# Kernel tuning notes

Measured on AMD Instinct MI355X. Metric: run time of the kernel, lower is better.

## Reference

```python
import jax, jax.numpy as jnp
import numpy as np

B, L, H, D = 2, 2048, 16, 64
HID = H * D
EPS = 1e-6


def setup_inputs() -> dict:
    key = jax.random.key(0)
    k1, k2, k3 = jax.random.split(key, 3)
    x = jax.random.normal(k1, (B, L, HID), dtype=jnp.float32)
    Wqkv = jax.random.normal(k2, (HID, 3 * HID), dtype=jnp.float32) * 0.02
    Wo = jax.random.normal(k3, (HID, HID), dtype=jnp.float32) * 0.02
    q_norm_w = jnp.ones((D,), dtype=jnp.float32)
    k_norm_w = jnp.ones((D,), dtype=jnp.float32)
    # real RoPE tables: (L, D/2)
    d2 = D // 2
    inv_freq = 1.0 / (10000.0 ** (np.arange(d2, dtype=np.float32) / d2))
    ang = np.arange(L, dtype=np.float32)[:, None] * inv_freq[None, :]
    cos = jnp.asarray(np.cos(ang), dtype=jnp.float32)
    sin = jnp.asarray(np.sin(ang), dtype=jnp.float32)
    return {"x": x, "Wqkv": Wqkv, "Wo": Wo, "q_norm_w": q_norm_w,
            "k_norm_w": k_norm_w, "cos": cos, "sin": sin}


def _rmsnorm(t, w, eps=EPS):
    # normalize over last (head_dim) axis
    var = jnp.mean(t * t, axis=-1, keepdims=True)
    return t * jax.lax.rsqrt(var + eps) * w


def _rope(t, cos, sin):
    # t: (B,H,L,D); cos,sin: (1,1,L,D/2)
    d2 = t.shape[-1] // 2
    t1, t2 = t[..., :d2], t[..., d2:]
    return jnp.concatenate([t1 * cos - t2 * sin, t1 * sin + t2 * cos], axis=-1)


def reference(x, Wqkv, Wo, q_norm_w, k_norm_w, cos, sin):
    Bx, Lx, _ = x.shape
    qkv = x @ Wqkv                                   # (B,L,3*HID)
    qkv = qkv.reshape(Bx, Lx, 3, H, D)
    q = jnp.transpose(qkv[:, :, 0], (0, 2, 1, 3))    # (B,H,L,D)
    k = jnp.transpose(qkv[:, :, 1], (0, 2, 1, 3))
    v = jnp.transpose(qkv[:, :, 2], (0, 2, 1, 3))
    q = _rmsnorm(q, q_norm_w)
    k = _rmsnorm(k, k_norm_w)
    c = cos[:Lx][None, None]                         # (1,1,L,D/2)
    s = sin[:Lx][None, None]
    q = _rope(q, c, s)
    k = _rope(k, c, s)
    scale = 1.0 / jnp.sqrt(jnp.float32(D))
    scores = jnp.einsum("bhqd,bhkd->bhqk", q, k) * scale
    causal = jnp.tril(jnp.ones((Lx, Lx), dtype=bool))
    scores = jnp.where(causal, scores, jnp.finfo(scores.dtype).min)
    attn = jax.nn.softmax(scores, axis=-1)
    out = jnp.einsum("bhqk,bhkd->bhqd", attn, v)     # (B,H,L,D)
    out = jnp.transpose(out, (0, 2, 1, 3)).reshape(Bx, Lx, HID)
    return out @ Wo
```

## Files before the change

### kernel.cpp

```cpp
#include <hip/hip_runtime.h>
#include <hip/hip_bf16.h>

typedef __attribute__((ext_vector_type(8))) short bh8;
typedef __attribute__((ext_vector_type(4))) float f4;

typedef unsigned short u16;
typedef unsigned int u32;

__device__ inline u16 f2b(float f) {
  __hip_bfloat16 h = __float2bfloat16(f);
  union { __hip_bfloat16 h; u16 u; } v; v.h = h; return v.u;
}
__device__ inline float b2f(u16 b) {
  union { u32 u; float f; } v; v.u = ((u32)b) << 16;
  return v.f;
}

__device__ __forceinline__ void gload16(const u16* g, u16* l) {
  __builtin_amdgcn_global_load_lds(
      (__attribute__((address_space(1))) void*)(g),
      (__attribute__((address_space(3))) void*)(l),
      16, 0, 0);
}

__global__ __launch_bounds__(256) void k_prep1(const float* __restrict__ x,
                                               const float* __restrict__ Wqkv,
                                               const float* __restrict__ Wo,
                                               u16* __restrict__ xb,
                                               u16* __restrict__ wqkvT,
                                               u16* __restrict__ woT) {
  int idx = blockIdx.x;
  if (idx < 4096) {
    int i = (idx * 256 + threadIdx.x) * 4;
    float4 v = *(const float4*)&x[i];
    ushort4 o;
    o.x = f2b(v.x); o.y = f2b(v.y); o.z = f2b(v.z); o.w = f2b(v.w);
    *(ushort4*)&xb[i] = o;
    return;
  }
  __shared__ u16 t[32][33];
  const float* W; u16* WT; int K, N, bxi, byi;
  if (idx < 7168) {
    int id2 = idx - 4096;
    W = Wqkv; WT = wqkvT; K = 1024; N = 3072;
    bxi = id2 % 96; byi = id2 / 96;
  } else {
    int id2 = idx - 7168;
    W = Wo; WT = woT; K = 1024; N = 1024;
    bxi = id2 & 31; byi = id2 >> 5;
  }
  int bx = bxi * 32, by = byi * 32;
  int xx = threadIdx.x & 31, yy = threadIdx.x >> 5;
  for (int j = 0; j < 4; ++j) {
    int r = yy + j * 8;
    t[r][xx] = f2b(W[(size_t)(by + r) * N + bx + xx]);
  }
  __syncthreads();
  for (int j = 0; j < 4; ++j) {
    int r = yy + j * 8;
    WT[(size_t)(bx + r) * K + by + xx] = t[xx][r];
  }
}

template <bool F32OUT>
__global__ __launch_bounds__(512, 2) void k_gemm256(const u16* __restrict__ A,
                                                    const u16* __restrict__ Bt,
                                                    void* __restrict__ Cout,
                                                    int M, int N, int K) {
  __shared__ u16 As[2][2][128 * 64];
  __shared__ u16 Bs[2][2][128 * 64];
  const int tid = threadIdx.x;
  const int lane = tid & 63, wid = tid >> 6;
  const int l15 = lane & 15, lg = lane >> 4;
  const int wm = wid >> 2, wn = wid & 3;

  int nwg = gridDim.x * gridDim.y;
  int bid = blockIdx.y * gridDim.x + blockIdx.x;
  int cpx = nwg >> 3;
  int swz = (bid & 7) * cpx + (bid >> 3);
  int bx = swz % gridDim.x, by = swz / gridDim.x;
  const int bm = bx * 256, bn = by * 256;

  f4 acc[8][4] = {};

  const int srow = wid * 16 + (lane >> 3);
  const int key0 = (lane >> 3) & 7;
  const int scol = ((lane & 7) ^ key0) * 8;

  const int nk = K >> 6;

#define STAGE256(T)                                                                   \
  {                                                                                   \
    int kb_ = (T) << 6; int bf_ = (T) & 1;                                            \
    _Pragma("unroll")                                                                 \
    for (int h = 0; h < 2; ++h) {                                                     \
      const u16* ga = A + (size_t)(bm + h * 128 + srow) * K + kb_ + scol;             \
      u16* la = &As[bf_][h][(wid * 16) * 64];                                         \
      gload16(ga, la);                                                                \
      gload16(ga + (size_t)8 * K, la + 8 * 64);                                       \
      const u16* gb = Bt + (size_t)(bn + h * 128 + srow) * K + kb_ + scol;            \
      u16* lb = &Bs[bf_][h][(wid * 16) * 64];                                         \
      gload16(gb, lb);                                                                \
      gload16(gb + (size_t)8 * K, lb + 8 * 64);                                       \
    }                                                                                 \
  }

#define QUAD256(T, MH, NH)                                                            \
  {                                                                                   \
    const u16* as_ = &As[(T) & 1][wm][0];                                             \
    const u16* bs_ = &Bs[(T) & 1][wn >> 1][0];                                        \
    bh8 a_[4][2], b_[2][2];                                                           \
    _Pragma("unroll")                                                                 \
    for (int i = 0; i < 4; ++i) {                                                     \
      int ar = ((MH) * 4 + i) * 16 + l15;                                             \
      _Pragma("unroll")                                                               \
      for (int kk = 0; kk < 2; ++kk)                                                  \
        a_[i][kk] = *(const bh8*)&as_[ar * 64 + (((kk * 4 + lg) ^ (ar & 7)) * 8)];    \
    }                                                                                 \
    _Pragma("unroll")                                                                 \
    for (int j = 0; j < 2; ++j) {                                                     \
      int br = (wn & 1) * 64 + ((NH) * 2 + j) * 16 + l15;                             \
      _Pragma("unroll")                                                               \
      for (int kk = 0; kk < 2; ++kk)                                                  \
        b_[j][kk] = *(const bh8*)&bs_[br * 64 + (((kk * 4 + lg) ^ (br & 7)) * 8)];    \
    }                                                                                 \
    asm volatile("s_waitcnt lgkmcnt(0)" ::: "memory");                                \
    __builtin_amdgcn_sched_barrier(0);                                                \
    __builtin_amdgcn_s_setprio(1);                                                    \
    _Pragma("unroll")                                                                 \
    for (int kk = 0; kk < 2; ++kk)                                                    \
      _Pragma("unroll")                                                               \
      for (int i = 0; i < 4; ++i)                                                     \
        _Pragma("unroll")                                                             \
        for (int j = 0; j < 2; ++j)                                                   \
          acc[(MH) * 4 + i][(NH) * 2 + j] = __builtin_amdgcn_mfma_f32_16x16x32_bf16(  \
              a_[i][kk], b_[j][kk], acc[(MH) * 4 + i][(NH) * 2 + j], 0, 0, 0);        \
    __builtin_amdgcn_s_setprio(0);                                                    \
  }

  STAGE256(0);
  asm volatile("s_waitcnt vmcnt(0)" ::: "memory");
  __builtin_amdgcn_s_barrier();

  for (int t = 0; t < nk; ++t) {
    if (t + 1 < nk) {
      STAGE256(t + 1);
      asm volatile("s_waitcnt vmcnt(8)" ::: "memory");
    } else {
      asm volatile("s_waitcnt vmcnt(0)" ::: "memory");
    }
    __builtin_amdgcn_s_barrier();
    __builtin_amdgcn_sched_barrier(0);
    QUAD256(t, 0, 0);
    QUAD256(t, 0, 1);
    QUAD256(t, 1, 0);
    QUAD256(t, 1, 1);
    __builtin_amdgcn_s_barrier();
  }
#undef STAGE256
#undef QUAD256

  for (int mf = 0; mf < 8; ++mf)
    for (int nf = 0; nf < 4; ++nf)
      for (int r = 0; r < 4; ++r) {
        int row = bm + wm * 128 + mf * 16 + lg * 4 + r;
        int col = bn + wn * 64 + nf * 16 + l15;
        float v = acc[mf][nf][r];
        if constexpr (F32OUT) ((float*)Cout)[(size_t)row * N + col] = v;
        else                  ((u16*)Cout)[(size_t)row * N + col]  = f2b(v);
      }
}

template <bool F32OUT>
__global__ __launch_bounds__(256) void k_gemm(const u16* __restrict__ A,
                                              const u16* __restrict__ Bt,
                                              void* __restrict__ Cout,
                                              int M, int N, int K) {
  __shared__ u16 As[2][128 * 64];
  __shared__ u16 Bs[2][128 * 64];
  const int tid = threadIdx.x;
  const int lane = tid & 63, wid = tid >> 6;
  const int l15 = lane & 15, lg = lane >> 4;
  const int bm = blockIdx.x * 128, bn = blockIdx.y * 128;
  const int wr = (wid >> 1) * 64, wc = (wid & 1) * 64;

  f4 acc[4][4] = {};

  const int srow = wid * 32 + (lane >> 3);
  const int scol = ((lane & 7) ^ ((lane >> 3) & 7)) * 8;
  const u16* gA = A  + (size_t)(bm + srow) * K + scol;
  const u16* gB = Bt + (size_t)(bn + srow) * K + scol;

  const int nk = K >> 6;

#define STAGE128(T)                                                \
  {                                                                \
    int kb_ = (T) << 6;                                            \
    const u16* ga = gA + kb_; const u16* gb = gB + kb_;            \
    u16* la = &As[(T) & 1][(wid * 32) * 64];                       \
    u16* lb = &Bs[(T) & 1][(wid * 32) * 64];                       \
    _Pragma("unroll")                                              \
    for (int c = 0; c < 4; ++c) {                                  \
      gload16(ga, la);                                             \
      gload16(gb, lb);                                             \
      ga += (size_t)8 * K; gb += (size_t)8 * K;                    \
      la += 8 * 64;        lb += 8 * 64;                           \
    }                                                              \
  }

  STAGE128(0);
  asm volatile("s_waitcnt vmcnt(0)" ::: "memory");
  __builtin_amdgcn_s_barrier();

  for (int t = 0; t < nk; ++t) {
    if (t + 1 < nk) {
      STAGE128(t + 1);
      asm volatile("s_waitcnt vmcnt(8)" ::: "memory");
    } else {
      asm volatile("s_waitcnt vmcnt(0)" ::: "memory");
    }
    __builtin_amdgcn_s_barrier();
    __builtin_amdgcn_sched_barrier(0);
    const u16* as = &As[t & 1][0];
    const u16* bs = &Bs[t & 1][0];
    #pragma unroll
    for (int kk = 0; kk < 2; ++kk) {
      bh8 a[4], b[4];
      #pragma unroll
      for (int m = 0; m < 4; ++m)
        a[m] = *(const bh8*)&as[(wr + m * 16 + l15) * 64 + (((kk * 4 + lg) ^ (l15 & 7)) * 8)];
      #pragma unroll
      for (int n = 0; n < 4; ++n)
        b[n] = *(const bh8*)&bs[(wc + n * 16 + l15) * 64 + (((kk * 4 + lg) ^ (l15 & 7)) * 8)];
      #pragma unroll
      for (int m = 0; m < 4; ++m)
        #pragma unroll
        for (int n = 0; n < 4; ++n)
          acc[m][n] = __builtin_amdgcn_mfma_f32_16x16x32_bf16(a[m], b[n], acc[m][n], 0, 0, 0);
    }
    __builtin_amdgcn_s_barrier();
  }
#undef STAGE128

  for (int m = 0; m < 4; ++m)
    for (int n = 0; n < 4; ++n)
      for (int r = 0; r < 4; ++r) {
        int row = bm + wr + m * 16 + lg * 4 + r;
        int col = bn + wc + n * 16 + l15;
        float v = acc[m][n][r];
        if constexpr (F32OUT) ((float*)Cout)[(size_t)row * N + col] = v;
        else                  ((u16*)Cout)[(size_t)row * N + col]  = f2b(v);
      }
}

__global__ __launch_bounds__(256) void k_prep2(const u16* __restrict__ qkv,
                                               const float* __restrict__ qw,
                                               const float* __restrict__ kw,
                                               const float* __restrict__ cosp,
                                               const float* __restrict__ sinp,
                                               u16* __restrict__ Q,
                                               u16* __restrict__ K,
                                               u16* __restrict__ Vt) {
  const float CSC = 0.125f * 1.44269504088896f;
  int idx = blockIdx.x;
  if (idx < 2048) {
    int wid = threadIdx.x >> 6, lane = threadIdx.x & 63;
    int gw = idx * 4 + wid;
    int isK = gw & 1;
    int bl = gw >> 1;
    int l = bl & 2047, b = bl >> 11;
    int h = lane >> 2, qd = lane & 3;
    const u16* src = qkv + (size_t)bl * 3072 + isK * 1024 + h * 64 + qd * 8;
    bh8 t1 = *(const bh8*)src;
    bh8 t2 = *(const bh8*)(src + 32);
    float a1[8], a2[8];
    float ss = 0.0f;
    #pragma unroll
    for (int j = 0; j < 8; ++j) {
      a1[j] = b2f((u16)t1[j]); a2[j] = b2f((u16)t2[j]);
      ss += a1[j] * a1[j] + a2[j] * a2[j];
    }
    ss += __shfl_xor(ss, 1, 64);
    ss += __shfl_xor(ss, 2, 64);
    float rr = rsqrtf(ss * (1.0f / 64.0f) + 1e-6f);
    const float* wt = isK ? kw : qw;
    float w1[8], w2[8], cc[8], sn[8];
    *(float4*)&w1[0] = *(const float4*)&wt[qd * 8];
    *(float4*)&w1[4] = *(const float4*)&wt[qd * 8 + 4];
    *(float4*)&w2[0] = *(const float4*)&wt[32 + qd * 8];
    *(float4*)&w2[4] = *(const float4*)&wt[32 + qd * 8 + 4];
    *(float4*)&cc[0] = *(const float4*)&cosp[l * 32 + qd * 8];
    *(float4*)&cc[4] = *(const float4*)&cosp[l * 32 + qd * 8 + 4];
    *(float4*)&sn[0] = *(const float4*)&sinp[l * 32 + qd * 8];
    *(float4*)&sn[4] = *(const float4*)&sinp[l * 32 + qd * 8 + 4];
    float scl = isK ? 1.0f : CSC;
    bh8 o1, o2;
    #pragma unroll
    for (int j = 0; j < 8; ++j) {
      float x1 = a1[j] * rr * w1[j];
      float x2 = a2[j] * rr * w2[j];
      o1[j] = (short)f2b((x1 * cc[j] - x2 * sn[j]) * scl);
      o2[j] = (short)f2b((x1 * sn[j] + x2 * cc[j]) * scl);
    }
    u16* dst = (isK ? K : Q) + ((size_t)(b * 16 + h) * 2048 + l) * 64 + qd * 8;
    *(bh8*)dst = o1;
    *(bh8*)(dst + 32) = o2;
  } else {
    __shared__ u16 tt[64][66];
    int v = idx - 2048;
    int bh = v >> 5, lt = v & 31;
    int b = bh >> 4, h = bh & 15;
    int lb = lt * 64;
    const u16* src = qkv + (size_t)b * 2048 * 3072 + 2048 + h * 64;
    int r0 = threadIdx.x >> 3, c0 = (threadIdx.x & 7) * 8;
    *(bh8*)&tt[r0][c0]      = *(const bh8*)&src[(size_t)(lb + r0) * 3072 + c0];
    *(bh8*)&tt[r0 + 32][c0] = *(const bh8*)&src[(size_t)(lb + r0 + 32) * 3072 + c0];
    __syncthreads();
    u16* dst = Vt + (size_t)bh * 64 * 2048;
    int d0 = threadIdx.x >> 3, l0 = (threadIdx.x & 7) * 8;
    bh8 o0, o1;
    #pragma unroll
    for (int j = 0; j < 8; ++j) {
      o0[j] = (short)tt[l0 + j][d0];
      o1[j] = (short)tt[l0 + j][d0 + 32];
    }
    *(bh8*)&dst[(size_t)d0 * 2048 + lb + l0]        = o0;
    *(bh8*)&dst[(size_t)(d0 + 32) * 2048 + lb + l0] = o1;
  }
}

__global__ __launch_bounds__(256, 3) void k_attn(const u16* __restrict__ Q,
                                                 const u16* __restrict__ K,
                                                 const u16* __restrict__ Vt,
                                                 u16* __restrict__ O,
                                                 u16* __restrict__ Opart,
                                                 float2* __restrict__ Ml) {
  __shared__ u16 Ks[2][64 * 64];
  __shared__ u16 Vs[2][64 * 64];
  __shared__ u16 Pl[4][32][64];

  const int wid = threadIdx.x >> 6, lane = threadIdx.x & 63;
  const int l15 = lane & 15, lg = lane >> 4;

  const int linear = (int)blockIdx.y * 46 + (int)blockIdx.x;
  const int xcd = linear & 7;
  const int rest = linear >> 3;
  const int bh = xcd * 4 + (rest & 3);
  const int chunkIdx = rest >> 2;
  const int b = bh >> 4, h = bh & 15;

  const int ctab[17] = {0,1,2,3,5,7,9,11,14,17,20,24,28,32,36,41,46};
  const int id = 45 - chunkIdx;
  int qt = 0;
  #pragma unroll
  for (int qq = 0; qq < 16; ++qq)
    if (id >= ctab[qq + 1]) qt = qq + 1;
  const int part = id - ctab[qt];
  const int ways = ctab[qt + 1] - ctab[qt];
  const int T = 2 * qt + 2;
  const int t0 = part * T / ways;
  const int t1 = (part + 1) * T / ways;
  const int slot = (ways == 1) ? -1 : bh * 43 + (id - 3);

  const int qb = qt * 128 + wid * 32;

  const u16* Qp = Q  + (size_t)bh * 2048 * 64;
  const u16* Kp = K  + (size_t)bh * 2048 * 64;
  const u16* Vp = Vt + (size_t)bh * 64 * 2048;

  const int sr0 = wid * 8 + (lane >> 3);
  const int sc  = lane & 7;

  bh8 aq[2][2];
  #pragma unroll
  for (int qi = 0; qi < 2; ++qi)
    #pragma unroll
    for (int hh = 0; hh < 2; ++hh)
      aq[qi][hh] = *(const bh8*)&Qp[(size_t)(qb + qi * 16 + l15) * 64 + hh * 32 + lg * 8];

  bh8 ones;
  #pragma unroll
  for (int j = 0; j < 8; ++j) ones[j] = (short)0x3F80;

  f4 acc[2][4] = {};
  float mrow[2] = {-1e30f, -1e30f};
  float lrow[2] = {0.0f, 0.0f};

  const int tmax = (qb + 31) >> 6;

  {
    int kb0 = t0 * 64;
    int r0 = sr0, r1 = 32 + sr0;
    gload16(Kp + (size_t)(kb0 + r0) * 64 + (size_t)((sc ^ (r0 & 7)) * 8), &Ks[t0 & 1][(wid * 8) * 64]);
    gload16(Kp + (size_t)(kb0 + r1) * 64 + (size_t)((sc ^ (r1 & 7)) * 8), &Ks[t0 & 1][(32 + wid * 8) * 64]);
    gload16(Vp + (size_t)r0 * 2048 + kb0 + (size_t)((sc ^ (r0 & 7)) * 8), &Vs[t0 & 1][(wid * 8) * 64]);
    gload16(Vp + (size_t)r1 * 2048 + kb0 + (size_t)((sc ^ (r1 & 7)) * 8), &Vs[t0 & 1][(32 + wid * 8) * 64]);
  }
  __syncthreads();

  for (int t = t0; t < t1; ++t) {
    if (t + 1 < t1) {
      int kb = (t + 1) * 64;
      int nb = (t + 1) & 1;
      int r0 = sr0, r1 = 32 + sr0;
      gload16(Kp + (size_t)(kb + r0) * 64 + (size_t)((sc ^ (r0 & 7)) * 8), &Ks[nb][(wid * 8) * 64]);
      gload16(Kp + (size_t)(kb + r1) * 64 + (size_t)((sc ^ (r1 & 7)) * 8), &Ks[nb][(32 + wid * 8) * 64]);
      gload16(Vp + (size_t)r0 * 2048 + kb + (size_t)((sc ^ (r0 & 7)) * 8), &Vs[nb][(wid * 8) * 64]);
      gload16(Vp + (size_t)r1 * 2048 + kb + (size_t)((sc ^ (r1 & 7)) * 8), &Vs[nb][(32 + wid * 8) * 64]);
    }
    if (t <= tmax) {
      const int kb = t * 64;
      const bool masked = (t == tmax);
      const u16* ks = &Ks[t & 1][0];
      const u16* vs = &Vs[t & 1][0];

      f4 sc4[4][2] = {};
      __builtin_amdgcn_s_setprio(1);
      #pragma unroll
      for (int kq = 0; kq < 4; ++kq) {
        int row = kq * 16 + l15;
        int cs = row & 7;
        bh8 ka0 = *(const bh8*)&ks[row * 64 + ((0 + lg) ^ cs) * 8];
        bh8 ka1 = *(const bh8*)&ks[row * 64 + ((4 + lg) ^ cs) * 8];
        #pragma unroll
        for (int qi = 0; qi < 2; ++qi) {
          sc4[kq][qi] = __builtin_amdgcn_mfma_f32_16x16x32_bf16(ka0, aq[qi][0], sc4[kq][qi], 0, 0, 0);
          sc4[kq][qi] = __builtin_amdgcn_mfma_f32_16x16x32_bf16(ka1, aq[qi][1], sc4[kq][qi], 0, 0, 0);
        }
      }
      __builtin_amdgcn_s_setprio(0);

      #pragma unroll
      for (int qi = 0; qi < 2; ++qi) {
        if (masked) {
          int q = qb + qi * 16 + l15;
          #pragma unroll
          for (int kq = 0; kq < 4; ++kq)
            #pragma unroll
            for (int r = 0; r < 4; ++r)
              if (kb + kq * 16 + lg * 4 + r > q) sc4[kq][qi][r] = -1e30f;
        }
        float mx = -1e30f;
        #pragma unroll
        for (int kq = 0; kq < 4; ++kq)
          #pragma unroll
          for (int r = 0; r < 4; ++r)
            mx = fmaxf(mx, sc4[kq][qi][r]);
        mx = fmaxf(mx, __shfl_xor(mx, 16, 64));
        mx = fmaxf(mx, __shfl_xor(mx, 32, 64));
        if (__any(mx > mrow[qi] + 8.0f)) {
          float mnew = fmaxf(mrow[qi], mx);
          float fac = exp2f(mrow[qi] - mnew);
          mrow[qi] = mnew;
          lrow[qi] *= fac;
          #pragma unroll
          for (int n = 0; n < 4; ++n)
            #pragma unroll
            for (int r = 0; r < 4; ++r) acc[qi][n][r] *= fac;
        }
        #pragma unroll
        for (int kq = 0; kq < 4; ++kq)
          #pragma unroll
          for (int r = 0; r < 4; ++r)
            sc4[kq][qi][r] = exp2f(sc4[kq][qi][r] - mrow[qi]);
      }

      char* plb = (char*)&Pl[wid][0][0];
      #pragma unroll
      for (int qi = 0; qi < 2; ++qi) {
        int row = qi * 16 + l15;
        #pragma unroll
        for (int kq = 0; kq < 4; ++kq) {
          ushort4 w4;
          w4.x = f2b(sc4[kq][qi][0]); w4.y = f2b(sc4[kq][qi][1]);
          w4.z = f2b(sc4[kq][qi][2]); w4.w = f2b(sc4[kq][qi][3]);
          int ch = (kq * 2 + (lg >> 1)) ^ (row & 7);
          *(ushort4*)(plb + row * 128 + ch * 16 + (lg & 1) * 8) = w4;
        }
      }
      asm volatile("s_waitcnt lgkmcnt(0)" ::: "memory");
      __builtin_amdgcn_sched_barrier(0);

      f4 sum0 = {}, sum1 = {};
      __builtin_amdgcn_s_setprio(1);
      #pragma unroll
      for (int g = 0; g < 2; ++g) {
        bh8 pb0 = *(const bh8*)(plb + l15 * 128 + (((g * 4 + lg) ^ (l15 & 7)) * 16));
        bh8 pb1 = *(const bh8*)(plb + (16 + l15) * 128 + (((g * 4 + lg) ^ (l15 & 7)) * 16));
        #pragma unroll
        for (int n = 0; n < 4; ++n) {
          int row = n * 16 + l15;
          bh8 va = *(const bh8*)&vs[row * 64 + (((g * 4 + lg) ^ (row & 7)) * 8)];
          acc[0][n] = __builtin_amdgcn_mfma_f32_16x16x32_bf16(va, pb0, acc[0][n], 0, 0, 0);
          acc[1][n] = __builtin_amdgcn_mfma_f32_16x16x32_bf16(va, pb1, acc[1][n], 0, 0, 0);
        }
        sum0 = __builtin_amdgcn_mfma_f32_16x16x32_bf16(ones, pb0, sum0, 0, 0, 0);
        sum1 = __builtin_amdgcn_mfma_f32_16x16x32_bf16(ones, pb1, sum1, 0, 0, 0);
      }
      __builtin_amdgcn_s_setprio(0);
      lrow[0] += sum0[0];
      lrow[1] += sum1[0];
    }
    __syncthreads();
  }

  if (slot < 0) {
    #pragma unroll
    for (int qi = 0; qi < 2; ++qi) {
      float inv = 1.0f / lrow[qi];
      int q = qb + qi * 16 + l15;
      #pragma unroll
      for (int n = 0; n < 4; ++n) {
        ushort4 w4;
        w4.x = f2b(acc[qi][n][0] * inv);
        w4.y = f2b(acc[qi][n][1] * inv);
        w4.z = f2b(acc[qi][n][2] * inv);
        w4.w = f2b(acc[qi][n][3] * inv);
        *(ushort4*)&O[((size_t)b * 2048 + q) * 1024 + h * 64 + n * 16 + lg * 4] = w4;
      }
    }
  } else {
    u16* op = Opart + (size_t)slot * 8192;
    #pragma unroll
    for (int qi = 0; qi < 2; ++qi) {
      int rloc = wid * 32 + qi * 16 + l15;
      #pragma unroll
      for (int n = 0; n < 4; ++n) {
        ushort4 w4;
        w4.x = f2b(acc[qi][n][0]); w4.y = f2b(acc[qi][n][1]);
        w4.z = f2b(acc[qi][n][2]); w4.w = f2b(acc[qi][n][3]);
        *(ushort4*)&op[(size_t)rloc * 64 + n * 16 + lg * 4] = w4;
      }
      if (lg == 0) Ml[slot * 128 + rloc] = make_float2(mrow[qi], lrow[qi]);
    }
  }
}

__global__ __launch_bounds__(256) void k_comb(const u16* __restrict__ Opart,
                                              const float2* __restrict__ Ml,
                                              u16* __restrict__ O) {
  const int ctab[17] = {0,1,2,3,5,7,9,11,14,17,20,24,28,32,36,41,46};
  int qt = 3 + (int)blockIdx.x;
  int bh = blockIdx.y;
  int b = bh >> 4, h = bh & 15;
  int ways = ctab[qt + 1] - ctab[qt];
  int base = bh * 43 + ctab[qt] - 3;
  int row = threadIdx.x >> 1;
  int db  = (threadIdx.x & 1) * 32;

  float2 ml[5]; float wgt[5];
  float M = -1e30f;
  #pragma unroll
  for (int w = 0; w < 5; ++w)
    if (w < ways) { ml[w] = Ml[(base + w) * 128 + row]; M = fmaxf(M, ml[w].x); }
  float l = 0.0f;
  #pragma unroll
  for (int w = 0; w < 5; ++w)
    if (w < ways) { wgt[w] = exp2f(ml[w].x - M); l += wgt[w] * ml[w].y; }
  float inv = 1.0f / l;

  u16* dst = O + ((size_t)b * 2048 + qt * 128 + row) * 1024 + h * 64 + db;
  #pragma unroll
  for (int j = 0; j < 32; j += 8) {
    float a[8] = {};
    #pragma unroll
    for (int w = 0; w < 5; ++w)
      if (w < ways) {
        bh8 v = *(const bh8*)&Opart[(size_t)(base + w) * 8192 + (size_t)row * 64 + db + j];
        #pragma unroll
        for (int e = 0; e < 8; ++e) a[e] += wgt[w] * b2f((u16)v[e]);
      }
    bh8 o;
    #pragma unroll
    for (int e = 0; e < 8; ++e) o[e] = (short)f2b(a[e] * inv);
    *(bh8*)&dst[j] = o;
  }
}

extern "C" void kernel_launch(void* const* d_in, const int* in_sizes, int n_in,
                              void* d_out, int out_size, void* d_ws, size_t ws_size,
                              hipStream_t stream) {
  (void)in_sizes; (void)n_in; (void)out_size; (void)ws_size;
  const float* x    = (const float*)d_in[0];
  const float* Wqkv = (const float*)d_in[1];
  const float* Wo   = (const float*)d_in[2];
  const float* qw   = (const float*)d_in[3];
  const float* kw   = (const float*)d_in[4];
  const float* cosp = (const float*)d_in[5];
  const float* sinp = (const float*)d_in[6];
  float* out = (float*)d_out;

  char* ws = (char*)d_ws;
  u16* xb    = (u16*)(ws);
  u16* wqkvT = (u16*)(ws + 8388608);
  u16* woT   = (u16*)(ws + 14680064);
  u16* qkv   = (u16*)(ws + 16777216);
  u16* Qb    = (u16*)(ws + 41943040);
  u16* Kb    = (u16*)(ws + 50331648);
  u16* Vtb   = (u16*)(ws + 58720256);
  u16* AO    = (u16*)(ws + 67108864);
  u16*    Opart = (u16*)(ws + 16777216);
  float2* Mlb   = (float2*)(ws + 16777216 + 22544384);

  k_prep1<<<8192, 256, 0, stream>>>(x, Wqkv, Wo, xb, wqkvT, woT);
  k_gemm256<false><<<dim3(16, 12), 512, 0, stream>>>(xb, wqkvT, qkv, 4096, 3072, 1024);
  k_prep2<<<3072, 256, 0, stream>>>(qkv, qw, kw, cosp, sinp, Qb, Kb, Vtb);
  k_attn<<<dim3(46, 32), 256, 0, stream>>>(Qb, Kb, Vtb, AO, Opart, Mlb);
  k_comb<<<dim3(13, 32), 256, 0, stream>>>(Opart, Mlb, AO);
  k_gemm<true><<<dim3(32, 8), 256, 0, stream>>>(AO, woT, out, 4096, 1024, 1024);
}
```

Before: 139.9 us.

## Enlarge attention query tile to 256 rows with two-pass softmax per warp

Each attention block now covers 256 query rows (64 per wave, handled in two passes of 32) instead of 128, so every K/V tile loaded into shared memory is reused by twice as many queries. The split-K chunk table, partial-output slots and the combine kernel are resized to match, and the Ml buffer moves to the start of the workspace. Fewer blocks mean less K/V global traffic. The costs are more registers per thread (Q fragments and accumulators double), which may hurt occupancy under the launch bound of 3, and coarser load balance across the causal triangle.

Result: slower. 160.5 us (+14.8%).

```diff
diff --git a/kernel.cpp b/kernel.cpp
--- a/kernel.cpp
+++ b/kernel.cpp
@@ -342,27 +342,27 @@
   const int wid = threadIdx.x >> 6, lane = threadIdx.x & 63;
   const int l15 = lane & 15, lg = lane >> 4;
 
-  const int linear = (int)blockIdx.y * 46 + (int)blockIdx.x;
+  const int linear = (int)blockIdx.y * 24 + (int)blockIdx.x;
   const int xcd = linear & 7;
   const int rest = linear >> 3;
   const int bh = xcd * 4 + (rest & 3);
   const int chunkIdx = rest >> 2;
   const int b = bh >> 4, h = bh & 15;
 
-  const int ctab[17] = {0,1,2,3,5,7,9,11,14,17,20,24,28,32,36,41,46};
-  const int id = 45 - chunkIdx;
+  const int ctab[9] = {0,1,3,5,8,11,15,19,24};
+  const int id = 23 - chunkIdx;
   int qt = 0;
   #pragma unroll
-  for (int qq = 0; qq < 16; ++qq)
+  for (int qq = 0; qq < 8; ++qq)
     if (id >= ctab[qq + 1]) qt = qq + 1;
   const int part = id - ctab[qt];
   const int ways = ctab[qt + 1] - ctab[qt];
-  const int T = 2 * qt + 2;
+  const int T = 4 * qt + 4;
   const int t0 = part * T / ways;
   const int t1 = (part + 1) * T / ways;
-  const int slot = (ways == 1) ? -1 : bh * 43 + (id - 3);
-
-  const int qb = qt * 128 + wid * 32;
+  const int slot = (ways == 1) ? -1 : bh * 23 + (id - 1);
+
+  const int qb = qt * 256 + wid * 64;
 
   const u16* Qp = Q  + (size_t)bh * 2048 * 64;
   const u16* Kp = K  + (size_t)bh * 2048 * 64;
@@ -371,9 +371,9 @@
   const int sr0 = wid * 8 + (lane >> 3);
   const int sc  = lane & 7;
 
-  bh8 aq[2][2];
+  bh8 aq[4][2];
   #pragma unroll
-  for (int qi = 0; qi < 2; ++qi)
+  for (int qi = 0; qi < 4; ++qi)
     #pragma unroll
     for (int hh = 0; hh < 2; ++hh)
       aq[qi][hh] = *(const bh8*)&Qp[(size_t)(qb + qi * 16 + l15) * 64 + hh * 32 + lg * 8];
@@ -382,11 +382,11 @@
   #pragma unroll
   for (int j = 0; j < 8; ++j) ones[j] = (short)0x3F80;
 
-  f4 acc[2][4] = {};
-  float mrow[2] = {-1e30f, -1e30f};
-  float lrow[2] = {0.0f, 0.0f};
-
-  const int tmax = (qb + 31) >> 6;
+  f4 acc[4][4] = {};
+  float mrow[4] = {-1e30f, -1e30f, -1e30f, -1e30f};
+  float lrow[4] = {0.0f, 0.0f, 0.0f, 0.0f};
+
+  const int tmax = (qb + 63) >> 6;
 
   {
     int kb0 = t0 * 64;
@@ -413,100 +413,107 @@
       const bool masked = (t == tmax);
       const u16* ks = &Ks[t & 1][0];
       const u16* vs = &Vs[t & 1][0];
-
-      f4 sc4[4][2] = {};
-      __builtin_amdgcn_s_setprio(1);
+      char* plb = (char*)&Pl[wid][0][0];
+
       #pragma unroll
-      for (int kq = 0; kq < 4; ++kq) {
-        int row = kq * 16 + l15;
-        int cs = row & 7;
-        bh8 ka0 = *(const bh8*)&ks[row * 64 + ((0 + lg) ^ cs) * 8];
-        bh8 ka1 = *(const bh8*)&ks[row * 64 + ((4 + lg) ^ cs) * 8];
+      for (int pass = 0; pass < 2; ++pass) {
+        const int qA = pass * 2, qB = pass * 2 + 1;
+
+        f4 sc4[4][2] = {};
+        __builtin_amdgcn_s_setprio(1);
         #pragma unroll
-        for (int qi = 0; qi < 2; ++qi) {
-          sc4[kq][qi] = __builtin_amdgcn_mfma_f32_16x16x32_bf16(ka0, aq[qi][0], sc4[kq][qi], 0, 0, 0);
-          sc4[kq][qi] = __builtin_amdgcn_mfma_f32_16x16x32_bf16(ka1, aq[qi][1], sc4[kq][qi], 0, 0, 0);
+        for (int kq = 0; kq < 4; ++kq) {
+          int row = kq * 16 + l15;
+          int cs = row & 7;
+          bh8 ka0 = *(const bh8*)&ks[row * 64 + ((0 + lg) ^ cs) * 8];
+          bh8 ka1 = *(const bh8*)&ks[row * 64 + ((4 + lg) ^ cs) * 8];
+          #pragma unroll
+          for (int jj = 0; jj < 2; ++jj) {
+            int qi = pass * 2 + jj;
+            sc4[kq][jj] = __builtin_amdgcn_mfma_f32_16x16x32_bf16(ka0, aq[qi][0], sc4[kq][jj], 0, 0, 0);
+            sc4[kq][jj] = __builtin_amdgcn_mfma_f32_16x16x32_bf16(ka1, aq[qi][1], sc4[kq][jj], 0, 0, 0);
+          }
         }
-      }
-      __builtin_amdgcn_s_setprio(0);
-
-      #pragma unroll
-      for (int qi = 0; qi < 2; ++qi) {
-        if (masked) {
-          int q = qb + qi * 16 + l15;
+        __builtin_amdgcn_s_setprio(0);
+
+        #pragma unroll
+        for (int jj = 0; jj < 2; ++jj) {
+          int qi = pass * 2 + jj;
+          if (masked) {
+            int q = qb + qi * 16 + l15;
+            #pragma unroll
+            for (int kq = 0; kq < 4; ++kq)
+              #pragma unroll
+              for (int r = 0; r < 4; ++r)
+                if (kb + kq * 16 + lg * 4 + r > q) sc4[kq][jj][r] = -1e30f;
+          }
+          float mx = -1e30f;
           #pragma unroll
           for (int kq = 0; kq < 4; ++kq)
             #pragma unroll
             for (int r = 0; r < 4; ++r)
-              if (kb + kq * 16 + lg * 4 + r > q) sc4[kq][qi][r] = -1e30f;
+              mx = fmaxf(mx, sc4[kq][jj][r]);
+          mx = fmaxf(mx, __shfl_xor(mx, 16, 64));
+          mx = fmaxf(mx, __shfl_xor(mx, 32, 64));
+          if (__any(mx > mrow[qi] + 8.0f)) {
+            float mnew = fmaxf(mrow[qi], mx);
+            float fac = exp2f(mrow[qi] - mnew);
+            mrow[qi] = mnew;
+            lrow[qi] *= fac;
+            #pragma unroll
+            for (int n = 0; n < 4; ++n)
+              #pragma unroll
+              for (int r = 0; r < 4; ++r) acc[qi][n][r] *= fac;
+          }
+          #pragma unroll
+          for (int kq = 0; kq < 4; ++kq)
+            #pragma unroll
+            for (int r = 0; r < 4; ++r)
+              sc4[kq][jj][r] = exp2f(sc4[kq][jj][r] - mrow[qi]);
         }
-        float mx = -1e30f;
+
         #pragma unroll
-        for (int kq = 0; kq < 4; ++kq)
+        for (int jj = 0; jj < 2; ++jj) {
+          int row = jj * 16 + l15;
           #pragma unroll
-          for (int r = 0; r < 4; ++r)
-            mx = fmaxf(mx, sc4[kq][qi][r]);
-        mx = fmaxf(mx, __shfl_xor(mx, 16, 64));
-        mx = fmaxf(mx, __shfl_xor(mx, 32, 64));
-        if (__any(mx > mrow[qi] + 8.0f)) {
-          float mnew = fmaxf(mrow[qi], mx);
-          float fac = exp2f(mrow[qi] - mnew);
-          mrow[qi] = mnew;
-          lrow[qi] *= fac;
+          for (int kq = 0; kq < 4; ++kq) {
+            ushort4 w4;
+            w4.x = f2b(sc4[kq][jj][0]); w4.y = f2b(sc4[kq][jj][1]);
+            w4.z = f2b(sc4[kq][jj][2]); w4.w = f2b(sc4[kq][jj][3]);
+            int ch = (kq * 2 + (lg >> 1)) ^ (row & 7);
+            *(ushort4*)(plb + row * 128 + ch * 16 + (lg & 1) * 8) = w4;
+          }
+        }
+        asm volatile("s_waitcnt lgkmcnt(0)" ::: "memory");
+        __builtin_amdgcn_sched_barrier(0);
+
+        f4 sum0 = {}, sum1 = {};
+        __builtin_amdgcn_s_setprio(1);
+        #pragma unroll
+        for (int g = 0; g < 2; ++g) {
+          bh8 pb0 = *(const bh8*)(plb + l15 * 128 + (((g * 4 + lg) ^ (l15 & 7)) * 16));
+          bh8 pb1 = *(const bh8*)(plb + (16 + l15) * 128 + (((g * 4 + lg) ^ (l15 & 7)) * 16));
           #pragma unroll
-          for (int n = 0; n < 4; ++n)
-            #pragma unroll
-            for (int r = 0; r < 4; ++r) acc[qi][n][r] *= fac;
+          for (int n = 0; n < 4; ++n) {
+            int row = n * 16 + l15;
+            bh8 va = *(const bh8*)&vs[row * 64 + (((g * 4 + lg) ^ (row & 7)) * 8)];
+            acc[qA][n] = __builtin_amdgcn_mfma_f32_16x16x32_bf16(va, pb0, acc[qA][n], 0, 0, 0);
+            acc[qB][n] = __builtin_amdgcn_mfma_f32_16x16x32_bf16(va, pb1, acc[qB][n], 0, 0, 0);
+          }
+          sum0 = __builtin_amdgcn_mfma_f32_16x16x32_bf16(ones, pb0, sum0, 0, 0, 0);
+          sum1 = __builtin_amdgcn_mfma_f32_16x16x32_bf16(ones, pb1, sum1, 0, 0, 0);
         }
-        #pragma unroll
-        for (int kq = 0; kq < 4; ++kq)
-          #pragma unroll
-          for (int r = 0; r < 4; ++r)
-            sc4[kq][qi][r] = exp2f(sc4[kq][qi][r] - mrow[qi]);
+        __builtin_amdgcn_s_setprio(0);
+        lrow[qA] += sum0[0];
+        lrow[qB] += sum1[0];
       }
-
-      char* plb = (char*)&Pl[wid][0][0];
-      #pragma unroll
-      for (int qi = 0; qi < 2; ++qi) {
-        int row = qi * 16 + l15;
-        #pragma unroll
-        for (int kq = 0; kq < 4; ++kq) {
-          ushort4 w4;
-          w4.x = f2b(sc4[kq][qi][0]); w4.y = f2b(sc4[kq][qi][1]);
-          w4.z = f2b(sc4[kq][qi][2]); w4.w = f2b(sc4[kq][qi][3]);
-          int ch = (kq * 2 + (lg >> 1)) ^ (row & 7);
-          *(ushort4*)(plb + row * 128 + ch * 16 + (lg & 1) * 8) = w4;
-        }
-      }
-      asm volatile("s_waitcnt lgkmcnt(0)" ::: "memory");
-      __builtin_amdgcn_sched_barrier(0);
-
-      f4 sum0 = {}, sum1 = {};
-      __builtin_amdgcn_s_setprio(1);
-      #pragma unroll
-      for (int g = 0; g < 2; ++g) {
-        bh8 pb0 = *(const bh8*)(plb + l15 * 128 + (((g * 4 + lg) ^ (l15 & 7)) * 16));
-        bh8 pb1 = *(const bh8*)(plb + (16 + l15) * 128 + (((g * 4 + lg) ^ (l15 & 7)) * 16));
-        #pragma unroll
-        for (int n = 0; n < 4; ++n) {
-          int row = n * 16 + l15;
-          bh8 va = *(const bh8*)&vs[row * 64 + (((g * 4 + lg) ^ (row & 7)) * 8)];
-          acc[0][n] = __builtin_amdgcn_mfma_f32_16x16x32_bf16(va, pb0, acc[0][n], 0, 0, 0);
-          acc[1][n] = __builtin_amdgcn_mfma_f32_16x16x32_bf16(va, pb1, acc[1][n], 0, 0, 0);
-        }
-        sum0 = __builtin_amdgcn_mfma_f32_16x16x32_bf16(ones, pb0, sum0, 0, 0, 0);
-        sum1 = __builtin_amdgcn_mfma_f32_16x16x32_bf16(ones, pb1, sum1, 0, 0, 0);
-      }
-      __builtin_amdgcn_s_setprio(0);
-      lrow[0] += sum0[0];
-      lrow[1] += sum1[0];
     }
     __syncthreads();
   }
 
   if (slot < 0) {
     #pragma unroll
-    for (int qi = 0; qi < 2; ++qi) {
+    for (int qi = 0; qi < 4; ++qi) {
       float inv = 1.0f / lrow[qi];
       int q = qb + qi * 16 + l15;
       #pragma unroll
@@ -520,10 +527,10 @@
       }
     }
   } else {
-    u16* op = Opart + (size_t)slot * 8192;
-    #pragma unroll
-    for (int qi = 0; qi < 2; ++qi) {
-      int rloc = wid * 32 + qi * 16 + l15;
+    u16* op = Opart + (size_t)slot * 16384;
+    #pragma unroll
+    for (int qi = 0; qi < 4; ++qi) {
+      int rloc = wid * 64 + qi * 16 + l15;
       #pragma unroll
       for (int n = 0; n < 4; ++n) {
         ushort4 w4;
@@ -531,7 +538,7 @@
         w4.z = f2b(acc[qi][n][2]); w4.w = f2b(acc[qi][n][3]);
         *(ushort4*)&op[(size_t)rloc * 64 + n * 16 + lg * 4] = w4;
       }
-      if (lg == 0) Ml[slot * 128 + rloc] = make_float2(mrow[qi], lrow[qi]);
+      if (lg == 0) Ml[slot * 256 + rloc] = make_float2(mrow[qi], lrow[qi]);
     }
   }
 }
@@ -539,34 +546,33 @@
 __global__ __launch_bounds__(256) void k_comb(const u16* __restrict__ Opart,
                                               const float2* __restrict__ Ml,
                                               u16* __restrict__ O) {
-  const int ctab[17] = {0,1,2,3,5,7,9,11,14,17,20,24,28,32,36,41,46};
-  int qt = 3 + (int)blockIdx.x;
+  const int ctab[9] = {0,1,3,5,8,11,15,19,24};
+  int qt = 1 + (int)blockIdx.x;
   int bh = blockIdx.y;
   int b = bh >> 4, h = bh & 15;
   int ways = ctab[qt + 1] - ctab[qt];
-  int base = bh * 43 + ctab[qt] - 3;
-  int row = threadIdx.x >> 1;
-  int db  = (threadIdx.x & 1) * 32;
+  int base = bh * 23 + ctab[qt] - 1;
+  int row = threadIdx.x;
 
   float2 ml[5]; float wgt[5];
   float M = -1e30f;
   #pragma unroll
   for (int w = 0; w < 5; ++w)
-    if (w < ways) { ml[w] = Ml[(base + w) * 128 + row]; M = fmaxf(M, ml[w].x); }
+    if (w < ways) { ml[w] = Ml[(base + w) * 256 + row]; M = fmaxf(M, ml[w].x); }
   float l = 0.0f;
   #pragma unroll
   for (int w = 0; w < 5; ++w)
     if (w < ways) { wgt[w] = exp2f(ml[w].x - M); l += wgt[w] * ml[w].y; }
   float inv = 1.0f / l;
 
-  u16* dst = O + ((size_t)b * 2048 + qt * 128 + row) * 1024 + h * 64 + db;
+  u16* dst = O + ((size_t)b * 2048 + qt * 256 + row) * 1024 + h * 64;
   #pragma unroll
-  for (int j = 0; j < 32; j += 8) {
+  for (int j = 0; j < 64; j += 8) {
     float a[8] = {};
     #pragma unroll
     for (int w = 0; w < 5; ++w)
       if (w < ways) {
-        bh8 v = *(const bh8*)&Opart[(size_t)(base + w) * 8192 + (size_t)row * 64 + db + j];
+        bh8 v = *(const bh8*)&Opart[(size_t)(base + w) * 16384 + (size_t)row * 64 + j];
         #pragma unroll
         for (int e = 0; e < 8; ++e) a[e] += wgt[w] * b2f((u16)v[e]);
       }
@@ -600,12 +606,12 @@
   u16* Vtb   = (u16*)(ws + 58720256);
   u16* AO    = (u16*)(ws + 67108864);
   u16*    Opart = (u16*)(ws + 16777216);
-  float2* Mlb   = (float2*)(ws + 16777216 + 22544384);
+  float2* Mlb   = (float2*)(ws);
 
   k_prep1<<<8192, 256, 0, stream>>>(x, Wqkv, Wo, xb, wqkvT, woT);
   k_gemm256<false><<<dim3(16, 12), 512, 0, stream>>>(xb, wqkvT, qkv, 4096, 3072, 1024);
   k_prep2<<<3072, 256, 0, stream>>>(qkv, qw, kw, cosp, sinp, Qb, Kb, Vtb);
-  k_attn<<<dim3(46, 32), 256, 0, stream>>>(Qb, Kb, Vtb, AO, Opart, Mlb);
-  k_comb<<<dim3(13, 32), 256, 0, stream>>>(Opart, Mlb, AO);
+  k_attn<<<dim3(24, 32), 256, 0, stream>>>(Qb, Kb, Vtb, AO, Opart, Mlb);
+  k_comb<<<dim3(7, 32), 256, 0, stream>>>(Opart, Mlb, AO);
   k_gemm<true><<<dim3(32, 8), 256, 0, stream>>>(AO, woT, out, 4096, 1024, 1024);
 }
```
